# Performance work log

Measured on AMD Instinct MI355X. Metric: run time of the kernel, lower is better.

## Reference

```python
import jax, jax.numpy as jnp
import numpy as np

N_NODES = 100000
N_EDGES = 1600000
D_IN = 128
D_OUT = 128


def setup_inputs() -> dict:
    key = jax.random.key(0)
    k1, k2, k3, k4, k5 = jax.random.split(key, 5)
    x = jax.random.normal(k1, (N_NODES, D_IN), dtype=jnp.float32)
    edge_row = jax.random.randint(k2, (N_EDGES,), 0, N_NODES, dtype=jnp.int32)
    edge_col = jax.random.randint(k3, (N_EDGES,), 0, N_NODES, dtype=jnp.int32)
    edge_vals = jax.random.uniform(k4, (N_EDGES,), dtype=jnp.float32)
    stdv = 1.0 / np.sqrt(D_OUT)
    weight = jax.random.uniform(k5, (D_IN, D_OUT), dtype=jnp.float32,
                                minval=-stdv, maxval=stdv)
    return {"x": x, "edge_row": edge_row, "edge_col": edge_col,
            "edge_vals": edge_vals, "weight": weight}


def reference(x, edge_row, edge_col, edge_vals, weight):
    # spmm(adj, x): gather source features, scale by edge weight, segment-sum to dst
    n = x.shape[0]
    msgs = x[edge_col] * edge_vals[:, None]          # [E, D_IN]
    agg = jax.ops.segment_sum(msgs, edge_row, num_segments=n)  # [N, D_IN]
    # dense weight matmul
    return agg @ weight                               # [N, D_OUT]
```

## Files before the change

### kernel.cpp

```cpp
#include <hip/hip_runtime.h>
#include <hip/hip_fp16.h>


#define N_NODES 100000
#define N_EDGES 1600000
#define DIM     128
#define BROWS   64
#define CB      1563
#define CAP     2048

#define OFF_CCNT   25600000
#define OFF_CSTART 25606400
#define OFF_CCUR   25612800
#define OFF_EBUF1  25619200

__global__ __launch_bounds__(256) void gemm_xw_kernel(
    const float* __restrict__ x,
    const float* __restrict__ W,
    __half*      __restrict__ y)
{
    __shared__ float As[32 * 32];
    __shared__ float Ws[32 * 128];

    const int t    = threadIdx.x;
    const int row0 = blockIdx.x * 32;
    const int r0   = (t >> 5) * 4;
    const int c0   = (t & 31) * 4;

    float acc[4][4];
#pragma unroll
    for (int i = 0; i < 4; ++i)
#pragma unroll
        for (int j = 0; j < 4; ++j) acc[i][j] = 0.f;

    for (int k0 = 0; k0 < 128; k0 += 32) {
        {
            int r  = t >> 3;
            int kp = t & 7;
            float4 a = *(const float4*)(x + (size_t)(row0 + r) * 128 + k0 + kp * 4);
            *(float4*)(As + r * 32 + kp * 4) = a;
        }
        {
            const float4* Wg = (const float4*)(W + (size_t)k0 * 128);
            float4* Wl = (float4*)Ws;
#pragma unroll
            for (int i = 0; i < 4; ++i) Wl[t + 256 * i] = Wg[t + 256 * i];
        }
        __syncthreads();

#pragma unroll
        for (int kk = 0; kk < 32; ++kk) {
            float4 w = *(const float4*)(Ws + kk * 128 + c0);
            float a0 = As[(r0 + 0) * 32 + kk];
            float a1 = As[(r0 + 1) * 32 + kk];
            float a2 = As[(r0 + 2) * 32 + kk];
            float a3 = As[(r0 + 3) * 32 + kk];
            acc[0][0] += a0 * w.x; acc[0][1] += a0 * w.y; acc[0][2] += a0 * w.z; acc[0][3] += a0 * w.w;
            acc[1][0] += a1 * w.x; acc[1][1] += a1 * w.y; acc[1][2] += a1 * w.z; acc[1][3] += a1 * w.w;
            acc[2][0] += a2 * w.x; acc[2][1] += a2 * w.y; acc[2][2] += a2 * w.z; acc[2][3] += a2 * w.w;
            acc[3][0] += a3 * w.x; acc[3][1] += a3 * w.y; acc[3][2] += a3 * w.z; acc[3][3] += a3 * w.w;
        }
        __syncthreads();
    }

#pragma unroll
    for (int i = 0; i < 4; ++i) {
        __half2 p0 = __floats2half2_rn(acc[i][0], acc[i][1]);
        __half2 p1 = __floats2half2_rn(acc[i][2], acc[i][3]);
        uint2 w;
        w.x = *(const unsigned*)&p0;
        w.y = *(const unsigned*)&p1;
        *(uint2*)(y + (size_t)(row0 + r0 + i) * 128 + c0) = w;
    }
}

__global__ __launch_bounds__(256) void zero_ccnt_kernel(unsigned* ccnt) {
    int i = blockIdx.x * 256 + threadIdx.x;
    if (i < CB) ccnt[i] = 0u;
}

__global__ __launch_bounds__(256) void coarse_hist_kernel(
    const int* __restrict__ erow, unsigned* __restrict__ ccnt)
{
    __shared__ unsigned lh[CB];
    const int t = threadIdx.x;
    const unsigned e0 = blockIdx.x * 8192u;
    for (int i = t; i < CB; i += 256) lh[i] = 0u;
    __syncthreads();
#pragma unroll 4
    for (int k = 0; k < 32; ++k) {
        unsigned e = e0 + k * 256u + t;
        if (e < N_EDGES) atomicAdd(&lh[(unsigned)erow[e] >> 6], 1u);
    }
    __syncthreads();
    for (int i = t; i < CB; i += 256) {
        unsigned h = lh[i];
        if (h) atomicAdd(&ccnt[i], h);
    }
}

__global__ __launch_bounds__(1024) void coarse_scan_kernel(
    const unsigned* __restrict__ ccnt,
    unsigned* __restrict__ cstart,
    unsigned* __restrict__ ccur)
{
    __shared__ unsigned wsum[16];
    const int t  = threadIdx.x;
    const int i0 = 2 * t;
    unsigned a  = (i0     < CB) ? ccnt[i0]     : 0u;
    unsigned bb = (i0 + 1 < CB) ? ccnt[i0 + 1] : 0u;
    unsigned s  = a + bb;
    unsigned inc = s;
#pragma unroll
    for (int d = 1; d < 64; d <<= 1) {
        unsigned o = __shfl_up(inc, d);
        if ((t & 63) >= d) inc += o;
    }
    if ((t & 63) == 63) wsum[t >> 6] = inc;
    __syncthreads();
    if (t == 0) {
        unsigned run = 0;
#pragma unroll
        for (int w = 0; w < 16; ++w) { unsigned sw = wsum[w]; wsum[w] = run; run += sw; }
        cstart[CB] = run;
    }
    __syncthreads();
    unsigned excl = inc - s + wsum[t >> 6];
    if (i0 < CB)     { cstart[i0]     = excl;     ccur[i0]     = excl;     }
    if (i0 + 1 < CB) { cstart[i0 + 1] = excl + a; ccur[i0 + 1] = excl + a; }
}

__global__ __launch_bounds__(256) void partition_kernel(
    const int*   __restrict__ erow,
    const int*   __restrict__ ecol,
    const float* __restrict__ eval,
    unsigned*    __restrict__ ccur,
    uint2*       __restrict__ ebuf1)
{
    __shared__ unsigned hist[CB];
    __shared__ unsigned gbase[CB];
    const int t = threadIdx.x;
    const unsigned e0 = blockIdx.x * 8192u;

    for (int i = t; i < CB; i += 256) hist[i] = 0u;
    __syncthreads();

#pragma unroll 4
    for (int k = 0; k < 32; ++k) {
        unsigned e = e0 + k * 256u + t;
        if (e < N_EDGES) atomicAdd(&hist[(unsigned)erow[e] >> 6], 1u);
    }
    __syncthreads();

    for (int i = t; i < CB; i += 256) {
        unsigned h = hist[i];
        gbase[i] = h ? atomicAdd(&ccur[i], h) : 0u;
        hist[i] = 0u;
    }
    __syncthreads();

#pragma unroll 4
    for (int k = 0; k < 32; ++k) {
        unsigned e = e0 + k * 256u + t;
        if (e < N_EDGES) {
            unsigned r = (unsigned)erow[e];
            unsigned b = r >> 6;
            unsigned rank = atomicAdd(&hist[b], 1u);
            ebuf1[gbase[b] + rank] =
                make_uint2(((r & 63u) << 17) | (unsigned)ecol[e],
                           __float_as_uint(eval[e]));
        }
    }
}

__global__ __launch_bounds__(256) void bucket_agg_kernel(
    const __half*   __restrict__ y,
    const unsigned* __restrict__ cstart,
    const uint2*    __restrict__ ebuf1,
    float*          __restrict__ out)
{
    __shared__ uint2    sorted[CAP];
    __shared__ unsigned hist[BROWS];
    __shared__ unsigned sstart[BROWS];
    __shared__ unsigned scur[BROWS];

    const int t    = threadIdx.x;
    const int b    = blockIdx.x;
    const int lane = t & 63;
    const int wv   = t >> 6;
    const unsigned lo = cstart[b];
    const unsigned hi = cstart[b + 1];
    const unsigned n  = hi - lo;
    const unsigned nchunks = n ? (n + CAP - 1) / CAP : 1u;

    for (unsigned c = 0; c < nchunks; ++c) {
        const unsigned base = lo + c * CAP;
        const unsigned m = (base < hi) ? ((hi - base < CAP) ? hi - base : CAP) : 0u;

        if (t < BROWS) hist[t] = 0u;
        __syncthreads();

        for (unsigned i = t; i < m; i += 256)
            atomicAdd(&hist[ebuf1[base + i].x >> 17], 1u);
        __syncthreads();

        if (t < 64) {
            unsigned v = hist[t];
            unsigned inc = v;
#pragma unroll
            for (int d = 1; d < 64; d <<= 1) {
                unsigned o = __shfl_up(inc, d);
                if (t >= d) inc += o;
            }
            unsigned excl = inc - v;
            sstart[t] = excl;
            scur[t]   = excl;
        }
        __syncthreads();

        for (unsigned i = t; i < m; i += 256) {
            uint2 rec = ebuf1[base + i];
            unsigned p = atomicAdd(&scur[rec.x >> 17], 1u);
            sorted[p] = rec;
        }
        __syncthreads();

        for (int r = wv; r < BROWS; r += 4) {
            int row = b * BROWS + r;
            if (row >= N_NODES) break;
            float ax, ay;
            if (c == 0) { ax = 0.f; ay = 0.f; }
            else {
                float2 p = *((const float2*)(out + (size_t)row * 128) + lane);
                ax = p.x; ay = p.y;
            }
            unsigned j = sstart[r], e = scur[r];
            for (; j + 4 <= e; j += 4) {
                uint2 r0 = sorted[j + 0];
                uint2 r1 = sorted[j + 1];
                uint2 r2 = sorted[j + 2];
                uint2 r3 = sorted[j + 3];
                const __half2 h0 = *((const __half2*)(y + (size_t)(r0.x & 0x1FFFFu) * 128) + lane);
                const __half2 h1 = *((const __half2*)(y + (size_t)(r1.x & 0x1FFFFu) * 128) + lane);
                const __half2 h2 = *((const __half2*)(y + (size_t)(r2.x & 0x1FFFFu) * 128) + lane);
                const __half2 h3 = *((const __half2*)(y + (size_t)(r3.x & 0x1FFFFu) * 128) + lane);
                float v0 = __uint_as_float(r0.y);
                float v1 = __uint_as_float(r1.y);
                float v2 = __uint_as_float(r2.y);
                float v3 = __uint_as_float(r3.y);
                float2 f0 = __half22float2(h0);
                float2 f1 = __half22float2(h1);
                float2 f2 = __half22float2(h2);
                float2 f3 = __half22float2(h3);
                ax = fmaf(f0.x, v0, ax); ay = fmaf(f0.y, v0, ay);
                ax = fmaf(f1.x, v1, ax); ay = fmaf(f1.y, v1, ay);
                ax = fmaf(f2.x, v2, ax); ay = fmaf(f2.y, v2, ay);
                ax = fmaf(f3.x, v3, ax); ay = fmaf(f3.y, v3, ay);
            }
            for (; j < e; ++j) {
                uint2 rr = sorted[j];
                const __half2 h = *((const __half2*)(y + (size_t)(rr.x & 0x1FFFFu) * 128) + lane);
                float v = __uint_as_float(rr.y);
                float2 f = __half22float2(h);
                ax = fmaf(f.x, v, ax); ay = fmaf(f.y, v, ay);
            }
            *((float2*)(out + (size_t)row * 128) + lane) = make_float2(ax, ay);
        }
        __syncthreads();
    }
}

extern "C" void kernel_launch(void* const* d_in, const int* in_sizes, int n_in,
                              void* d_out, int out_size, void* d_ws, size_t ws_size,
                              hipStream_t stream) {
    const float* x    = (const float*)d_in[0];
    const int*   erow = (const int*)d_in[1];
    const int*   ecol = (const int*)d_in[2];
    const float* eval = (const float*)d_in[3];
    const float* W    = (const float*)d_in[4];
    float* out = (float*)d_out;

    char* ws = (char*)d_ws;
    __half*   y      = (__half*)  (ws);
    unsigned* ccnt   = (unsigned*)(ws + OFF_CCNT);
    unsigned* cstart = (unsigned*)(ws + OFF_CSTART);
    unsigned* ccur   = (unsigned*)(ws + OFF_CCUR);
    uint2*    ebuf1  = (uint2*)   (ws + OFF_EBUF1);

    gemm_xw_kernel<<<N_NODES / 32, 256, 0, stream>>>(x, W, y);
    zero_ccnt_kernel<<<(CB + 255) / 256, 256, 0, stream>>>(ccnt);
    coarse_hist_kernel<<<196, 256, 0, stream>>>(erow, ccnt);
    coarse_scan_kernel<<<1, 1024, 0, stream>>>(ccnt, cstart, ccur);
    partition_kernel<<<196, 256, 0, stream>>>(erow, ecol, eval, ccur, ebuf1);
    bucket_agg_kernel<<<CB, 256, 0, stream>>>(y, cstart, ebuf1, out);
}
```

Baseline: 293.2 us.

## Halve bucket size, double partition blocks, stage bucket records in LDS

Shrinks each coarse bucket from 64 to 32 destination rows, which doubles the number of aggregation blocks. It also halves the edges handled per partition and histogram block, so those kernels launch twice as many blocks. The aggregation kernel now copies each chunk of edge records into shared memory once and reuses that copy for the local sort, instead of reading the records from global memory twice. The cost is more atomics on the coarse counters, a larger scan, and smaller per-row batches in the aggregation kernel.

Result: no change. 293.2 us (+0.0%).

```diff
diff --git a/kernel.cpp b/kernel.cpp
--- a/kernel.cpp
+++ b/kernel.cpp
@@ -5,14 +5,16 @@
 #define N_NODES 100000
 #define N_EDGES 1600000
 #define DIM     128
-#define BROWS   64
-#define CB      1563
-#define CAP     2048
+#define BROWS   32
+#define CB      3125
+#define CAP     1024
+#define EPB     4096
+#define PBLK    392
 
 #define OFF_CCNT   25600000
-#define OFF_CSTART 25606400
-#define OFF_CCUR   25612800
-#define OFF_EBUF1  25619200
+#define OFF_CSTART 25612800
+#define OFF_CCUR   25625600
+#define OFF_EBUF1  25638400
 
 __global__ __launch_bounds__(256) void gemm_xw_kernel(
     const float* __restrict__ x,
@@ -84,13 +86,13 @@
 {
     __shared__ unsigned lh[CB];
     const int t = threadIdx.x;
-    const unsigned e0 = blockIdx.x * 8192u;
+    const unsigned e0 = blockIdx.x * (unsigned)EPB;
     for (int i = t; i < CB; i += 256) lh[i] = 0u;
     __syncthreads();
 #pragma unroll 4
-    for (int k = 0; k < 32; ++k) {
+    for (int k = 0; k < EPB / 256; ++k) {
         unsigned e = e0 + k * 256u + t;
-        if (e < N_EDGES) atomicAdd(&lh[(unsigned)erow[e] >> 6], 1u);
+        if (e < N_EDGES) atomicAdd(&lh[(unsigned)erow[e] >> 5], 1u);
     }
     __syncthreads();
     for (int i = t; i < CB; i += 256) {
@@ -106,10 +108,12 @@
 {
     __shared__ unsigned wsum[16];
     const int t  = threadIdx.x;
-    const int i0 = 2 * t;
-    unsigned a  = (i0     < CB) ? ccnt[i0]     : 0u;
-    unsigned bb = (i0 + 1 < CB) ? ccnt[i0 + 1] : 0u;
-    unsigned s  = a + bb;
+    const int i0 = 4 * t;
+    unsigned v0 = (i0 + 0 < CB) ? ccnt[i0 + 0] : 0u;
+    unsigned v1 = (i0 + 1 < CB) ? ccnt[i0 + 1] : 0u;
+    unsigned v2 = (i0 + 2 < CB) ? ccnt[i0 + 2] : 0u;
+    unsigned v3 = (i0 + 3 < CB) ? ccnt[i0 + 3] : 0u;
+    unsigned s  = v0 + v1 + v2 + v3;
     unsigned inc = s;
 #pragma unroll
     for (int d = 1; d < 64; d <<= 1) {
@@ -126,8 +130,10 @@
     }
     __syncthreads();
     unsigned excl = inc - s + wsum[t >> 6];
-    if (i0 < CB)     { cstart[i0]     = excl;     ccur[i0]     = excl;     }
-    if (i0 + 1 < CB) { cstart[i0 + 1] = excl + a; ccur[i0 + 1] = excl + a; }
+    if (i0 + 0 < CB) { cstart[i0 + 0] = excl;                ccur[i0 + 0] = excl;                }
+    if (i0 + 1 < CB) { cstart[i0 + 1] = excl + v0;           ccur[i0 + 1] = excl + v0;           }
+    if (i0 + 2 < CB) { cstart[i0 + 2] = excl + v0 + v1;      ccur[i0 + 2] = excl + v0 + v1;      }
+    if (i0 + 3 < CB) { cstart[i0 + 3] = excl + v0 + v1 + v2; ccur[i0 + 3] = excl + v0 + v1 + v2; }
 }
 
 __global__ __launch_bounds__(256) void partition_kernel(
@@ -140,15 +146,15 @@
     __shared__ unsigned hist[CB];
     __shared__ unsigned gbase[CB];
     const int t = threadIdx.x;
-    const unsigned e0 = blockIdx.x * 8192u;
+    const unsigned e0 = blockIdx.x * (unsigned)EPB;
 
     for (int i = t; i < CB; i += 256) hist[i] = 0u;
     __syncthreads();
 
 #pragma unroll 4
-    for (int k = 0; k < 32; ++k) {
+    for (int k = 0; k < EPB / 256; ++k) {
         unsigned e = e0 + k * 256u + t;
-        if (e < N_EDGES) atomicAdd(&hist[(unsigned)erow[e] >> 6], 1u);
+        if (e < N_EDGES) atomicAdd(&hist[(unsigned)erow[e] >> 5], 1u);
     }
     __syncthreads();
 
@@ -160,14 +166,14 @@
     __syncthreads();
 
 #pragma unroll 4
-    for (int k = 0; k < 32; ++k) {
+    for (int k = 0; k < EPB / 256; ++k) {
         unsigned e = e0 + k * 256u + t;
         if (e < N_EDGES) {
             unsigned r = (unsigned)erow[e];
-            unsigned b = r >> 6;
+            unsigned b = r >> 5;
             unsigned rank = atomicAdd(&hist[b], 1u);
             ebuf1[gbase[b] + rank] =
-                make_uint2(((r & 63u) << 17) | (unsigned)ecol[e],
+                make_uint2(((r & 31u) << 17) | (unsigned)ecol[e],
                            __float_as_uint(eval[e]));
         }
     }
@@ -179,6 +185,7 @@
     const uint2*    __restrict__ ebuf1,
     float*          __restrict__ out)
 {
+    __shared__ uint2    raw[CAP];
     __shared__ uint2    sorted[CAP];
     __shared__ unsigned hist[BROWS];
     __shared__ unsigned sstart[BROWS];
@@ -190,22 +197,25 @@
     const int wv   = t >> 6;
     const unsigned lo = cstart[b];
     const unsigned hi = cstart[b + 1];
-    const unsigned n  = hi - lo;
+    const unsigned n  = (hi > lo) ? (hi - lo) : 0u;
     const unsigned nchunks = n ? (n + CAP - 1) / CAP : 1u;
 
     for (unsigned c = 0; c < nchunks; ++c) {
         const unsigned base = lo + c * CAP;
-        const unsigned m = (base < hi) ? ((hi - base < CAP) ? hi - base : CAP) : 0u;
+        const unsigned m = (n > c * CAP) ? (((n - c * CAP) < CAP) ? (n - c * CAP) : CAP) : 0u;
 
         if (t < BROWS) hist[t] = 0u;
         __syncthreads();
 
-        for (unsigned i = t; i < m; i += 256)
-            atomicAdd(&hist[ebuf1[base + i].x >> 17], 1u);
+        for (unsigned i = t; i < m; i += 256) {
+            uint2 rec = ebuf1[base + i];
+            raw[i] = rec;
+            atomicAdd(&hist[rec.x >> 17], 1u);
+        }
         __syncthreads();
 
         if (t < 64) {
-            unsigned v = hist[t];
+            unsigned v = (t < BROWS) ? hist[t] : 0u;
             unsigned inc = v;
 #pragma unroll
             for (int d = 1; d < 64; d <<= 1) {
@@ -213,13 +223,12 @@
                 if (t >= d) inc += o;
             }
             unsigned excl = inc - v;
-            sstart[t] = excl;
-            scur[t]   = excl;
+            if (t < BROWS) { sstart[t] = excl; scur[t] = excl; }
         }
         __syncthreads();
 
         for (unsigned i = t; i < m; i += 256) {
-            uint2 rec = ebuf1[base + i];
+            uint2 rec = raw[i];
             unsigned p = atomicAdd(&scur[rec.x >> 17], 1u);
             sorted[p] = rec;
         }
@@ -289,8 +298,8 @@
 
     gemm_xw_kernel<<<N_NODES / 32, 256, 0, stream>>>(x, W, y);
     zero_ccnt_kernel<<<(CB + 255) / 256, 256, 0, stream>>>(ccnt);
-    coarse_hist_kernel<<<196, 256, 0, stream>>>(erow, ccnt);
+    coarse_hist_kernel<<<PBLK, 256, 0, stream>>>(erow, ccnt);
     coarse_scan_kernel<<<1, 1024, 0, stream>>>(ccnt, cstart, ccur);
-    partition_kernel<<<196, 256, 0, stream>>>(erow, ecol, eval, ccur, ebuf1);
+    partition_kernel<<<PBLK, 256, 0, stream>>>(erow, ecol, eval, ccur, ebuf1);
     bucket_agg_kernel<<<CB, 256, 0, stream>>>(y, cstart, ebuf1, out);
 }
```
